# Optimization experiments

Measured on AMD Instinct MI355X. Metric: run time of the kernel, lower is better.

Reference implementation:

```python
import jax, jax.numpy as jnp
import numpy as np

EPS = 1e-12  # torch F.normalize eps


def _l2_normalize(v, axis):
    n = jnp.linalg.norm(v, axis=axis, keepdims=True)
    return v / jnp.maximum(n, EPS)


def setup_inputs() -> dict:
    key = jax.random.key(0)
    k1, k2, k3, k4 = jax.random.split(key, 4)
    B, D, H = 4096, 1024, 16384
    x = jax.random.normal(k1, (B, D), dtype=jnp.float32)
    # kaiming_uniform(a=sqrt(5)) on [H, D]: bound = sqrt(6 / ((1+5) * D)) = 1/sqrt(D)
    bound_e = 1.0 / np.sqrt(D)
    encoder = jax.random.uniform(k2, (H, D), dtype=jnp.float32, minval=-bound_e, maxval=bound_e)
    # nn.Linear(H, D): weight [D, H] kaiming_uniform(a=sqrt(5)) -> bound 1/sqrt(H); bias uniform(+-1/sqrt(H))
    bound_d = 1.0 / np.sqrt(H)
    decoder_w = jax.random.uniform(k3, (D, H), dtype=jnp.float32, minval=-bound_d, maxval=bound_d)
    decoder_b = jax.random.uniform(k4, (D,), dtype=jnp.float32, minval=-bound_d, maxval=bound_d)
    return {"x": x, "encoder": encoder, "decoder_w": decoder_w, "decoder_b": decoder_b}


def reference(x, encoder, decoder_w, decoder_b):
    TOPK = 32
    w = _l2_normalize(encoder, axis=1)          # [H, D]
    x_n = _l2_normalize(x, axis=-1)             # [B, D]
    cos_sim = jnp.einsum('bd,hd->bh', x_n, w)   # [B, H]
    cos_sim = jnp.clip(cos_sim, -1.0, 1.0)
    acts = 2.0 - jnp.sqrt(2.0 - 2.0 * cos_sim)  # [B, H]
    topk_vals, topk_idx = jax.lax.top_k(acts, TOPK)  # [B, K]
    B = acts.shape[0]
    rows = jnp.arange(B)[:, None]               # [B, 1]
    latent = jnp.zeros_like(acts).at[rows, topk_idx].set(topk_vals)  # [B, H]
    recon = latent @ decoder_w.T + decoder_b    # [B, D]
    return recon, latent
```

## Files before the change

kernel.cpp:

```cpp
#include <hip/hip_runtime.h>


#define DEV static __device__ __forceinline__

constexpr int Bm_ = 4096;
constexpr int Dd_ = 1024;
constexpr int Hh_ = 16384;
constexpr int K3_ = 3072;
constexpr int TOPK = 32;
constexpr int CMAX = 64;

typedef __bf16 bf16x8 __attribute__((ext_vector_type(8)));
typedef float f32x4 __attribute__((ext_vector_type(4)));

DEV unsigned short f2bf_rne(float f) {
    unsigned u = __float_as_uint(f);
    unsigned r = u + 0x7FFFu + ((u >> 16) & 1u);
    return (unsigned short)(r >> 16);
}
DEV float bf2f(unsigned short h) { return __uint_as_float(((unsigned)h) << 16); }

__global__ __launch_bounds__(256) void prep_split(const float* __restrict__ src,
                                                  unsigned short* __restrict__ dst,
                                                  int dup_off, int lo_off) {
    int row = blockIdx.x, t = threadIdx.x;
    float4 v = reinterpret_cast<const float4*>(src + (size_t)row * Dd_)[t];
    float ss = v.x * v.x + v.y * v.y + v.z * v.z + v.w * v.w;
    for (int off = 1; off < 64; off <<= 1) ss += __shfl_xor(ss, off);
    __shared__ float red[4];
    __shared__ float s_rn;
    if ((t & 63) == 0) red[t >> 6] = ss;
    __syncthreads();
    if (t == 0) s_rn = 1.0f / fmaxf(sqrtf(red[0] + red[1] + red[2] + red[3]), 1e-12f);
    __syncthreads();
    float rn = s_rn;
    float vv[4] = {v.x, v.y, v.z, v.w};
    unsigned short h[4], l[4];
#pragma unroll
    for (int j = 0; j < 4; j++) {
        float xn = vv[j] * rn;
        unsigned short hb = f2bf_rne(xn);
        h[j] = hb;
        l[j] = f2bf_rne(xn - bf2f(hb));
    }
    ushort4 hv = make_ushort4(h[0], h[1], h[2], h[3]);
    ushort4 lv = make_ushort4(l[0], l[1], l[2], l[3]);
    unsigned short* bp = dst + (size_t)row * K3_ + t * 4;
    *reinterpret_cast<ushort4*>(bp) = hv;
    *reinterpret_cast<ushort4*>(bp + dup_off) = hv;
    *reinterpret_cast<ushort4*>(bp + lo_off) = lv;
}

#define GBM 256
#define GBN 256
#define GBK 64
#define NT 48

DEV void gload_lds16(const void* g, void* l) {
    __builtin_amdgcn_global_load_lds(
        (const __attribute__((address_space(1))) void*)g,
        (__attribute__((address_space(3))) void*)l, 16, 0, 0);
}

#define STG_A(bb, h, ko) do {                                                   \
    gload_lds16(Ab + aoff[h][0] + (ko), &As[bb][h][lofs[0]]);                   \
    gload_lds16(Ab + aoff[h][1] + (ko), &As[bb][h][lofs[1]]); } while (0)
#define STG_B(bb, h, ko) do {                                                   \
    gload_lds16(Bb + boff[h][0] + (ko), &Bs[bb][h][lofs[0]]);                   \
    gload_lds16(Bb + boff[h][1] + (ko), &Bs[bb][h][lofs[1]]); } while (0)

#define LD_AF(bb, mh) do { _Pragma("unroll") for (int mm = 0; mm < 4; mm++)     \
    _Pragma("unroll") for (int ks = 0; ks < 2; ks++)                            \
        af[mm][ks] = *reinterpret_cast<const bf16x8*>(                          \
            &As[bb][mh][(wm * 64 + mm * 16 + l15) * 64 +                        \
                        (((ks * 4) + g4) ^ l7) * 8]); } while (0)
#define LD_BF(dst, bb, nh) do { _Pragma("unroll") for (int nn = 0; nn < 2; nn++) \
    _Pragma("unroll") for (int ks = 0; ks < 2; ks++)                            \
        dst[nn][ks] = *reinterpret_cast<const bf16x8*>(                         \
            &Bs[bb][nh][(wn * 32 + nn * 16 + l15) * 64 +                        \
                        (((ks * 4) + g4) ^ l7) * 8]); } while (0)

#define MFMA16(mh, nh, BF) do {                                                 \
    __builtin_amdgcn_s_setprio(1);                                              \
    _Pragma("unroll") for (int mm = 0; mm < 4; mm++)                            \
    _Pragma("unroll") for (int nn = 0; nn < 2; nn++)                            \
    _Pragma("unroll") for (int ks = 0; ks < 2; ks++)                            \
        acc[(mh) * 4 + mm][(nh) * 2 + nn] = __builtin_amdgcn_mfma_f32_16x16x32_bf16( \
            af[mm][ks], BF[nn][ks], acc[(mh) * 4 + mm][(nh) * 2 + nn], 0, 0, 0); \
    __builtin_amdgcn_s_setprio(0); } while (0)

#define VMW4 asm volatile("s_waitcnt vmcnt(4)" ::: "memory")
#define LGKM0 do { asm volatile("s_waitcnt lgkmcnt(0)" ::: "memory");           \
                   __builtin_amdgcn_sched_barrier(0); } while (0)
#define BAR __builtin_amdgcn_s_barrier()

__global__ __launch_bounds__(512, 2) void gemm_acts(const unsigned short* __restrict__ A,
                                                    const unsigned short* __restrict__ Bp,
                                                    float* __restrict__ acts) {
    __shared__ unsigned short As[2][2][128 * 64];
    __shared__ unsigned short Bs[2][2][128 * 64];
    const int t = threadIdx.x;
    const int lane = t & 63, w = t >> 6;
    const int wm = w >> 2, wn = w & 3;
    const int l15 = lane & 15, g4 = lane >> 4, l7 = lane & 7;

    const int bid = blockIdx.x;
    const int wg = (bid & 7) * 128 + (bid >> 3);
    const int mb = wg & 15, nb = wg >> 4;
    const unsigned short* Ab = A + (size_t)(mb * GBM) * K3_;
    const unsigned short* Bb = Bp + (size_t)(nb * GBN) * K3_;

    int aoff[2][2], boff[2][2];
    int lofs[2];
#pragma unroll
    for (int i = 0; i < 2; i++) {
        int p = t + i * 512;
        int lr = p >> 3;
        int sg = (p & 7) ^ (lr & 7);
        lofs[i] = p * 8;
#pragma unroll
        for (int h = 0; h < 2; h++) {
            aoff[h][i] = ((lr >> 6) * 128 + h * 64 + (lr & 63)) * K3_ + sg * 8;
            boff[h][i] = ((lr >> 5) * 64 + h * 32 + (lr & 31)) * K3_ + sg * 8;
        }
    }

    f32x4 acc[8][4] = {};
    bf16x8 af[4][2], bfA[2][2], bfB[2][2];

    STG_A(0, 0, 0);
    STG_B(0, 0, 0);
    STG_B(0, 1, 0);
    STG_A(0, 1, 0);

    for (int kt = 0; kt < NT; ++kt) {
        const int cur = kt & 1, nxt = cur ^ 1;
        const int ko = (kt < NT - 1 ? kt + 1 : kt) * GBK;
        VMW4; BAR;
        LD_AF(cur, 0);
        LD_BF(bfA, cur, 0);
        STG_A(nxt, 0, ko);
        BAR; LGKM0;
        MFMA16(0, 0, bfA);
        VMW4; BAR;
        LD_BF(bfB, cur, 1);
        STG_B(nxt, 0, ko);
        BAR; LGKM0;
        MFMA16(0, 1, bfB);
        VMW4; BAR;
        LD_AF(cur, 1);
        STG_B(nxt, 1, ko);
        BAR; LGKM0;
        MFMA16(1, 0, bfA);
        BAR;
        STG_A(nxt, 1, ko);
        BAR;
        MFMA16(1, 1, bfB);
    }

    const int col0 = nb * GBN + wn * 64 + l15;
    const int row0 = mb * GBM + wm * 128 + g4 * 4;
#pragma unroll
    for (int m = 0; m < 8; m++)
#pragma unroll
        for (int n = 0; n < 4; n++)
#pragma unroll
            for (int j = 0; j < 4; j++) {
                float c = acc[m][n][j];
                c = fminf(fmaxf(c, -1.0f), 1.0f);
                float a2 = 2.0f - sqrtf(fmaxf(2.0f - 2.0f * c, 0.0f));
                acts[(size_t)(row0 + m * 16 + j) * Hh_ + (col0 + n * 16)] = a2;
            }
}

__global__ __launch_bounds__(256) void topk_refine_recon(float* __restrict__ latent,
                                                         const float* __restrict__ x,
                                                         const float* __restrict__ enc,
                                                         const float* __restrict__ dwT,
                                                         const float* __restrict__ dbias,
                                                         float* __restrict__ recon) {
    int b = blockIdx.x, t = threadIdx.x;
    float* rowp = latent + (size_t)b * Hh_;
    unsigned u[64];
#pragma unroll
    for (int q = 0; q < 16; q++) {
        float4 v = reinterpret_cast<const float4*>(rowp)[q * 256 + t];
        u[q * 4 + 0] = __float_as_uint(v.x);
        u[q * 4 + 1] = __float_as_uint(v.y);
        u[q * 4 + 2] = __float_as_uint(v.z);
        u[q * 4 + 3] = __float_as_uint(v.w);
    }
    __shared__ int red[4];
    __shared__ unsigned s_cnt;
    __shared__ int s_cidx[CMAX];
    __shared__ float sx[Dd_];
    __shared__ double s_redd[4];
    __shared__ double s_nx2;
    __shared__ double cvals[CMAX];
    __shared__ int cjd[CMAX];
    __shared__ float sv[TOPK];
    __shared__ int si[TOPK];

    unsigned lo = 0u, hi = 0x40000001u;
    for (int it = 0; it < 31; ++it) {
        unsigned mid = lo + ((hi - lo) >> 1);
        int c = 0;
#pragma unroll
        for (int j = 0; j < 64; j++) c += (u[j] >= mid) ? 1 : 0;
        for (int off = 1; off < 64; off <<= 1) c += __shfl_xor(c, off);
        if ((t & 63) == 0) red[t >> 6] = c;
        __syncthreads();
        c = red[0] + red[1] + red[2] + red[3];
        __syncthreads();
        if (c >= TOPK) {
            lo = mid;
            if (c <= 48) break;
        } else {
            hi = mid;
        }
    }
    unsigned cthr = __float_as_uint(fmaxf(__uint_as_float(lo) - 1e-4f, 0.0f));
    if (t == 0) s_cnt = 0;
    __syncthreads();
    float4 z = {0.0f, 0.0f, 0.0f, 0.0f};
#pragma unroll
    for (int q = 0; q < 16; q++) {
#pragma unroll
        for (int k = 0; k < 4; k++) {
            if (u[q * 4 + k] >= cthr) {
                unsigned slot = atomicAdd(&s_cnt, 1u);
                if (slot < CMAX) s_cidx[slot] = (q * 256 + t) * 4 + k;
            }
        }
        reinterpret_cast<float4*>(rowp)[q * 256 + t] = z;
    }
    float4 xv = reinterpret_cast<const float4*>(x + (size_t)b * Dd_)[t];
    reinterpret_cast<float4*>(sx)[t] = xv;
    double ss = (double)xv.x * xv.x + (double)xv.y * xv.y +
                (double)xv.z * xv.z + (double)xv.w * xv.w;
    for (int off = 1; off < 64; off <<= 1) ss += __shfl_xor(ss, off);
    if ((t & 63) == 0) s_redd[t >> 6] = ss;
    __syncthreads();
    if (t == 0) s_nx2 = s_redd[0] + s_redd[1] + s_redd[2] + s_redd[3];
    __syncthreads();
    double nx = fmax(sqrt(s_nx2), 1e-12);
    int C = (int)min(s_cnt, (unsigned)CMAX);

    int grp = t >> 5, lr = t & 31;
    for (int c = grp; c < C; c += 8) {
        int j = s_cidx[c];
        const float* wr = enc + (size_t)j * Dd_;
        double xw = 0.0, w2 = 0.0;
#pragma unroll
        for (int q = 0; q < 8; q++) {
            float4 wvv = reinterpret_cast<const float4*>(wr)[q * 32 + lr];
            float4 xs  = reinterpret_cast<const float4*>(sx)[q * 32 + lr];
            xw += (double)xs.x * wvv.x + (double)xs.y * wvv.y +
                  (double)xs.z * wvv.z + (double)xs.w * wvv.w;
            w2 += (double)wvv.x * wvv.x + (double)wvv.y * wvv.y +
                  (double)wvv.z * wvv.z + (double)wvv.w * wvv.w;
        }
        for (int off = 1; off < 32; off <<= 1) {
            xw += __shfl_xor(xw, off);
            w2 += __shfl_xor(w2, off);
        }
        if (lr == 0) {
            double nw = fmax(sqrt(w2), 1e-12);
            double cs = fmin(fmax(xw / (nx * nw), -1.0), 1.0);
            cvals[c] = 2.0 - sqrt(fmax(2.0 - 2.0 * cs, 0.0));
            cjd[c] = j;
        }
    }
    __syncthreads();
    if (t < C) {
        double v = cvals[t];
        int j = cjd[t];
        int rank = 0;
        for (int c2 = 0; c2 < C; c2++) {
            double v2 = cvals[c2];
            rank += (v2 > v) || (v2 == v && cjd[c2] < j);
        }
        if (rank < TOPK) {
            latent[(size_t)b * Hh_ + j] = (float)v;
            sv[rank] = (float)v;
            si[rank] = j;
        }
    }
    __syncthreads();
    float4 acc = reinterpret_cast<const float4*>(dbias)[t];
#pragma unroll 8
    for (int k = 0; k < TOPK; k++) {
        float v = sv[k];
        float4 wv = reinterpret_cast<const float4*>(dwT + (size_t)si[k] * Dd_)[t];
        acc.x += v * wv.x; acc.y += v * wv.y; acc.z += v * wv.z; acc.w += v * wv.w;
    }
    reinterpret_cast<float4*>(recon + (size_t)b * Dd_)[t] = acc;
}

__global__ __launch_bounds__(256) void transpose_dw(const float* __restrict__ dw,
                                                    float* __restrict__ dwT) {
    __shared__ float tile[32][33];
    int hb = blockIdx.x * 32, db = blockIdx.y * 32;
    int tx = threadIdx.x & 31, ty = threadIdx.x >> 5;
#pragma unroll
    for (int j = 0; j < 4; j++)
        tile[ty + 8 * j][tx] = dw[(size_t)(db + ty + 8 * j) * Hh_ + hb + tx];
    __syncthreads();
#pragma unroll
    for (int j = 0; j < 4; j++)
        dwT[(size_t)(hb + ty + 8 * j) * Dd_ + db + tx] = tile[tx][ty + 8 * j];
}

extern "C" void kernel_launch(void* const* d_in, const int* in_sizes, int n_in,
                              void* d_out, int out_size, void* d_ws, size_t ws_size,
                              hipStream_t stream) {
    const float* x   = (const float*)d_in[0];
    const float* enc = (const float*)d_in[1];
    const float* dw  = (const float*)d_in[2];
    const float* db  = (const float*)d_in[3];

    float* recon  = (float*)d_out;
    float* latent = (float*)d_out + (size_t)Bm_ * Dd_;

    char* ws = (char*)d_ws;
    unsigned short* Ap = (unsigned short*)ws;
    unsigned short* Bp = (unsigned short*)(ws + 25165824);
    float* dwT = (float*)ws;

    prep_split<<<Bm_, 256, 0, stream>>>(x, Ap, 1024, 2048);
    prep_split<<<Hh_, 256, 0, stream>>>(enc, Bp, 2048, 1024);
    gemm_acts<<<(Bm_ / GBM) * (Hh_ / GBN), 512, 0, stream>>>(Ap, Bp, latent);
    transpose_dw<<<dim3(Hh_ / 32, Dd_ / 32), 256, 0, stream>>>(dw, dwT);
    topk_refine_recon<<<Bm_, 256, 0, stream>>>(latent, x, enc, dwT, db, recon);
}
```

Before: 1.116 ms.

## Restructure GEMM LDS staging and shortcut top-k refinement when exactly K candidates

The GEMM drops the split half-tile staging with many barriers and per-phase vmcnt waits. It now uses whole 256x64 A and B tiles loaded in two bursts per k-step, with a single vmcnt(0) wait plus one barrier per iteration, and interleaves the fragment loads with the MFMAs. The top-k kernel keeps bisecting until exactly 32 candidates pass the threshold. In that case it takes the bf16-split GEMM values directly and skips the fp64 recompute of cosine similarity against the encoder rows. This trades fewer synchronisations for a deeper wait on each load, and on the fast path gives up the exact recomputed values and tie handling.

```diff
diff --git a/kernel.cpp b/kernel.cpp
--- a/kernel.cpp
+++ b/kernel.cpp
@@ -62,23 +62,16 @@
         (__attribute__((address_space(3))) void*)l, 16, 0, 0);
 }
 
-#define STG_A(bb, h, ko) do {                                                   \
-    gload_lds16(Ab + aoff[h][0] + (ko), &As[bb][h][lofs[0]]);                   \
-    gload_lds16(Ab + aoff[h][1] + (ko), &As[bb][h][lofs[1]]); } while (0)
-#define STG_B(bb, h, ko) do {                                                   \
-    gload_lds16(Bb + boff[h][0] + (ko), &Bs[bb][h][lofs[0]]);                   \
-    gload_lds16(Bb + boff[h][1] + (ko), &Bs[bb][h][lofs[1]]); } while (0)
-
 #define LD_AF(bb, mh) do { _Pragma("unroll") for (int mm = 0; mm < 4; mm++)     \
     _Pragma("unroll") for (int ks = 0; ks < 2; ks++)                            \
         af[mm][ks] = *reinterpret_cast<const bf16x8*>(                          \
-            &As[bb][mh][(wm * 64 + mm * 16 + l15) * 64 +                        \
-                        (((ks * 4) + g4) ^ l7) * 8]); } while (0)
+            &As[bb][(wm * 128 + (mh) * 64 + mm * 16 + l15) * 64 +               \
+                    (((ks * 4) + g4) ^ l7) * 8]); } while (0)
 #define LD_BF(dst, bb, nh) do { _Pragma("unroll") for (int nn = 0; nn < 2; nn++) \
     _Pragma("unroll") for (int ks = 0; ks < 2; ks++)                            \
         dst[nn][ks] = *reinterpret_cast<const bf16x8*>(                         \
-            &Bs[bb][nh][(wn * 32 + nn * 16 + l15) * 64 +                        \
-                        (((ks * 4) + g4) ^ l7) * 8]); } while (0)
+            &Bs[bb][(wn * 64 + (nh) * 32 + nn * 16 + l15) * 64 +                \
+                    (((ks * 4) + g4) ^ l7) * 8]); } while (0)
 
 #define MFMA16(mh, nh, BF) do {                                                 \
     __builtin_amdgcn_s_setprio(1);                                              \
@@ -89,16 +82,13 @@
             af[mm][ks], BF[nn][ks], acc[(mh) * 4 + mm][(nh) * 2 + nn], 0, 0, 0); \
     __builtin_amdgcn_s_setprio(0); } while (0)
 
-#define VMW4 asm volatile("s_waitcnt vmcnt(4)" ::: "memory")
-#define LGKM0 do { asm volatile("s_waitcnt lgkmcnt(0)" ::: "memory");           \
-                   __builtin_amdgcn_sched_barrier(0); } while (0)
-#define BAR __builtin_amdgcn_s_barrier()
+#define SBAR __builtin_amdgcn_sched_barrier(0)
 
 __global__ __launch_bounds__(512, 2) void gemm_acts(const unsigned short* __restrict__ A,
                                                     const unsigned short* __restrict__ Bp,
                                                     float* __restrict__ acts) {
-    __shared__ unsigned short As[2][2][128 * 64];
-    __shared__ unsigned short Bs[2][2][128 * 64];
+    __shared__ unsigned short As[2][GBM * GBK];
+    __shared__ unsigned short Bs[2][GBN * GBK];
     const int t = threadIdx.x;
     const int lane = t & 63, w = t >> 6;
     const int wm = w >> 2, wn = w & 3;
@@ -110,51 +100,47 @@
     const unsigned short* Ab = A + (size_t)(mb * GBM) * K3_;
     const unsigned short* Bb = Bp + (size_t)(nb * GBN) * K3_;
 
-    int aoff[2][2], boff[2][2];
-    int lofs[2];
-#pragma unroll
-    for (int i = 0; i < 2; i++) {
+    const unsigned short* asrc[4];
+    const unsigned short* bsrc[4];
+    unsigned adst[4];
+#pragma unroll
+    for (int i = 0; i < 4; i++) {
         int p = t + i * 512;
-        int lr = p >> 3;
-        int sg = (p & 7) ^ (lr & 7);
-        lofs[i] = p * 8;
-#pragma unroll
-        for (int h = 0; h < 2; h++) {
-            aoff[h][i] = ((lr >> 6) * 128 + h * 64 + (lr & 63)) * K3_ + sg * 8;
-            boff[h][i] = ((lr >> 5) * 64 + h * 32 + (lr & 31)) * K3_ + sg * 8;
-        }
+        int r = p >> 3;
+        int sg = (p & 7) ^ (r & 7);
+        asrc[i] = Ab + (size_t)r * K3_ + sg * 8;
+        bsrc[i] = Bb + (size_t)r * K3_ + sg * 8;
+        adst[i] = (unsigned)p * 8;
     }
 
     f32x4 acc[8][4] = {};
     bf16x8 af[4][2], bfA[2][2], bfB[2][2];
 
-    STG_A(0, 0, 0);
-    STG_B(0, 0, 0);
-    STG_B(0, 1, 0);
-    STG_A(0, 1, 0);
+#pragma unroll
+    for (int i = 0; i < 4; i++) gload_lds16(asrc[i], &As[0][adst[i]]);
+#pragma unroll
+    for (int i = 0; i < 4; i++) gload_lds16(bsrc[i], &Bs[0][adst[i]]);
 
     for (int kt = 0; kt < NT; ++kt) {
         const int cur = kt & 1, nxt = cur ^ 1;
-        const int ko = (kt < NT - 1 ? kt + 1 : kt) * GBK;
-        VMW4; BAR;
+        const int ko = (kt < NT - 1 ? (kt + 1) : kt) * GBK;
+        asm volatile("s_waitcnt vmcnt(0)" ::: "memory");
+        SBAR;
+        __builtin_amdgcn_s_barrier();
         LD_AF(cur, 0);
         LD_BF(bfA, cur, 0);
-        STG_A(nxt, 0, ko);
-        BAR; LGKM0;
+        LD_BF(bfB, cur, 1);
+#pragma unroll
+        for (int i = 0; i < 4; i++) gload_lds16(asrc[i] + ko, &As[nxt][adst[i]]);
+        SBAR;
         MFMA16(0, 0, bfA);
-        VMW4; BAR;
-        LD_BF(bfB, cur, 1);
-        STG_B(nxt, 0, ko);
-        BAR; LGKM0;
         MFMA16(0, 1, bfB);
-        VMW4; BAR;
+        SBAR;
         LD_AF(cur, 1);
-        STG_B(nxt, 1, ko);
-        BAR; LGKM0;
+#pragma unroll
+        for (int i = 0; i < 4; i++) gload_lds16(bsrc[i] + ko, &Bs[nxt][adst[i]]);
+        SBAR;
         MFMA16(1, 0, bfA);
-        BAR;
-        STG_A(nxt, 1, ko);
-        BAR;
         MFMA16(1, 1, bfB);
     }
 
@@ -193,6 +179,7 @@
     __shared__ int red[4];
     __shared__ unsigned s_cnt;
     __shared__ int s_cidx[CMAX];
+    __shared__ float s_cval[CMAX];
     __shared__ float sx[Dd_];
     __shared__ double s_redd[4];
     __shared__ double s_nx2;
@@ -214,12 +201,12 @@
         __syncthreads();
         if (c >= TOPK) {
             lo = mid;
-            if (c <= 48) break;
+            if (c == TOPK) break;
         } else {
             hi = mid;
         }
     }
-    unsigned cthr = __float_as_uint(fmaxf(__uint_as_float(lo) - 1e-4f, 0.0f));
+    unsigned cthr = __float_as_uint(fmaxf(__uint_as_float(lo) - 1e-5f, 0.0f));
     if (t == 0) s_cnt = 0;
     __syncthreads();
     float4 z = {0.0f, 0.0f, 0.0f, 0.0f};
@@ -229,61 +216,74 @@
         for (int k = 0; k < 4; k++) {
             if (u[q * 4 + k] >= cthr) {
                 unsigned slot = atomicAdd(&s_cnt, 1u);
-                if (slot < CMAX) s_cidx[slot] = (q * 256 + t) * 4 + k;
+                if (slot < CMAX) {
+                    s_cidx[slot] = (q * 256 + t) * 4 + k;
+                    s_cval[slot] = __uint_as_float(u[q * 4 + k]);
+                }
             }
         }
         reinterpret_cast<float4*>(rowp)[q * 256 + t] = z;
     }
-    float4 xv = reinterpret_cast<const float4*>(x + (size_t)b * Dd_)[t];
-    reinterpret_cast<float4*>(sx)[t] = xv;
-    double ss = (double)xv.x * xv.x + (double)xv.y * xv.y +
-                (double)xv.z * xv.z + (double)xv.w * xv.w;
-    for (int off = 1; off < 64; off <<= 1) ss += __shfl_xor(ss, off);
-    if ((t & 63) == 0) s_redd[t >> 6] = ss;
-    __syncthreads();
-    if (t == 0) s_nx2 = s_redd[0] + s_redd[1] + s_redd[2] + s_redd[3];
-    __syncthreads();
-    double nx = fmax(sqrt(s_nx2), 1e-12);
+    __syncthreads();
     int C = (int)min(s_cnt, (unsigned)CMAX);
 
-    int grp = t >> 5, lr = t & 31;
-    for (int c = grp; c < C; c += 8) {
-        int j = s_cidx[c];
-        const float* wr = enc + (size_t)j * Dd_;
-        double xw = 0.0, w2 = 0.0;
-#pragma unroll
-        for (int q = 0; q < 8; q++) {
-            float4 wvv = reinterpret_cast<const float4*>(wr)[q * 32 + lr];
-            float4 xs  = reinterpret_cast<const float4*>(sx)[q * 32 + lr];
-            xw += (double)xs.x * wvv.x + (double)xs.y * wvv.y +
-                  (double)xs.z * wvv.z + (double)xs.w * wvv.w;
-            w2 += (double)wvv.x * wvv.x + (double)wvv.y * wvv.y +
-                  (double)wvv.z * wvv.z + (double)wvv.w * wvv.w;
-        }
-        for (int off = 1; off < 32; off <<= 1) {
-            xw += __shfl_xor(xw, off);
-            w2 += __shfl_xor(w2, off);
-        }
-        if (lr == 0) {
-            double nw = fmax(sqrt(w2), 1e-12);
-            double cs = fmin(fmax(xw / (nx * nw), -1.0), 1.0);
-            cvals[c] = 2.0 - sqrt(fmax(2.0 - 2.0 * cs, 0.0));
-            cjd[c] = j;
-        }
-    }
-    __syncthreads();
-    if (t < C) {
-        double v = cvals[t];
-        int j = cjd[t];
-        int rank = 0;
-        for (int c2 = 0; c2 < C; c2++) {
-            double v2 = cvals[c2];
-            rank += (v2 > v) || (v2 == v && cjd[c2] < j);
-        }
-        if (rank < TOPK) {
-            latent[(size_t)b * Hh_ + j] = (float)v;
-            sv[rank] = (float)v;
-            si[rank] = j;
+    if (C == TOPK) {
+        if (t < TOPK) {
+            sv[t] = s_cval[t];
+            si[t] = s_cidx[t];
+            latent[(size_t)b * Hh_ + s_cidx[t]] = s_cval[t];
+        }
+    } else {
+        float4 xv = reinterpret_cast<const float4*>(x + (size_t)b * Dd_)[t];
+        reinterpret_cast<float4*>(sx)[t] = xv;
+        double ss = (double)xv.x * xv.x + (double)xv.y * xv.y +
+                    (double)xv.z * xv.z + (double)xv.w * xv.w;
+        for (int off = 1; off < 64; off <<= 1) ss += __shfl_xor(ss, off);
+        if ((t & 63) == 0) s_redd[t >> 6] = ss;
+        __syncthreads();
+        if (t == 0) s_nx2 = s_redd[0] + s_redd[1] + s_redd[2] + s_redd[3];
+        __syncthreads();
+        double nx = fmax(sqrt(s_nx2), 1e-12);
+
+        int grp = t >> 5, lr = t & 31;
+        for (int c = grp; c < C; c += 8) {
+            int j = s_cidx[c];
+            const float* wr = enc + (size_t)j * Dd_;
+            double xw = 0.0, w2 = 0.0;
+#pragma unroll
+            for (int q = 0; q < 8; q++) {
+                float4 wvv = reinterpret_cast<const float4*>(wr)[q * 32 + lr];
+                float4 xs  = reinterpret_cast<const float4*>(sx)[q * 32 + lr];
+                xw += (double)xs.x * wvv.x + (double)xs.y * wvv.y +
+                      (double)xs.z * wvv.z + (double)xs.w * wvv.w;
+                w2 += (double)wvv.x * wvv.x + (double)wvv.y * wvv.y +
+                      (double)wvv.z * wvv.z + (double)wvv.w * wvv.w;
+            }
+            for (int off = 1; off < 32; off <<= 1) {
+                xw += __shfl_xor(xw, off);
+                w2 += __shfl_xor(w2, off);
+            }
+            if (lr == 0) {
+                double nw = fmax(sqrt(w2), 1e-12);
+                double cs = fmin(fmax(xw / (nx * nw), -1.0), 1.0);
+                cvals[c] = 2.0 - sqrt(fmax(2.0 - 2.0 * cs, 0.0));
+                cjd[c] = j;
+            }
+        }
+        __syncthreads();
+        if (t < C) {
+            double v = cvals[t];
+            int j = cjd[t];
+            int rank = 0;
+            for (int c2 = 0; c2 < C; c2++) {
+                double v2 = cvals[c2];
+                rank += (v2 > v) || (v2 == v && cjd[c2] < j);
+            }
+            if (rank < TOPK) {
+                latent[(size_t)b * Hh_ + j] = (float)v;
+                sv[rank] = (float)v;
+                si[rank] = j;
+            }
         }
     }
     __syncthreads();
```

Result: faster. 947.2 us (-15.1%).
